# Optimization experiments

Measured on AMD Instinct MI355X. Metric: run time of the kernel, lower is better.

Reference implementation:

```python
import jax, jax.numpy as jnp
import numpy as np

NUM_EMBED = 1024
NUM_HEADS = 16
BLOCK_SIZE = 2048


def setup_inputs() -> dict:
    key = jax.random.key(0)
    k1, k2, k3, k4, k5 = jax.random.split(key, 5)
    C = NUM_EMBED
    s = 1.0 / np.sqrt(C)
    x = jax.random.normal(k1, (2, BLOCK_SIZE, C), dtype=jnp.float32)
    # nn.Linear params: weight (out,in), bias (out,)
    w_attn = jax.random.uniform(k2, (3 * C, C), minval=-s, maxval=s, dtype=jnp.float32)
    b_attn = jax.random.uniform(k3, (3 * C,), minval=-s, maxval=s, dtype=jnp.float32)
    w_proj = jax.random.uniform(k4, (C, C), minval=-s, maxval=s, dtype=jnp.float32)
    b_proj = jax.random.uniform(k5, (C,), minval=-s, maxval=s, dtype=jnp.float32)
    return {"x": x, "w_attn": w_attn, "b_attn": b_attn, "w_proj": w_proj, "b_proj": b_proj}


def reference(x, w_attn, b_attn, w_proj, b_proj):
    B, T, C = x.shape
    H = NUM_HEADS
    D = C // H
    kqv = jnp.einsum('btc,oc->bto', x, w_attn) + b_attn  # (B,T,3C)
    # Original code splits as K, Q, V in that order.
    K, Q, V = jnp.split(kqv, 3, axis=2)
    K = K.reshape(B, T, H, D).transpose(0, 2, 1, 3)  # (B,H,T,D)
    Q = Q.reshape(B, T, H, D).transpose(0, 2, 1, 3)
    V = V.reshape(B, T, H, D).transpose(0, 2, 1, 3)
    aff = jnp.einsum('bhqd,bhkd->bhqk', Q, K) * (D ** -0.5)  # (B,H,T,T)
    causal = jnp.tril(jnp.ones((T, T), dtype=bool))
    aff = jnp.where(causal[None, None], aff, jnp.float32(-jnp.inf))
    wei = jax.nn.softmax(aff, axis=-1)
    attn = jnp.einsum('bhqk,bhkd->bhqd', wei, V)
    attn = attn.transpose(0, 2, 1, 3).reshape(B, T, C)
    out = jnp.einsum('btc,oc->bto', attn, w_proj) + b_proj
    return out
```

## Files before the change

### kernel.cpp

```cpp
#include <hip/hip_runtime.h>
#include <hip/hip_bf16.h>
#include <cstdint>

typedef __attribute__((ext_vector_type(8))) short bf16x8;
typedef __attribute__((ext_vector_type(4))) float f32x4;
typedef __attribute__((ext_vector_type(4))) uint16_t u16x4;

__device__ __forceinline__ uint16_t f2b(float f) {
  union { float f; uint32_t i; } v; v.f = f;
  return (uint16_t)((v.i + 0x7FFFu + ((v.i >> 16) & 1u)) >> 16);
}

#define GLDS16(g, l) __builtin_amdgcn_global_load_lds( \
    (const __attribute__((address_space(1))) void*)(g), \
    (__attribute__((address_space(3))) void*)(l), 16, 0, 0)

__global__ __launch_bounds__(256) void cvt_all(
    const float* __restrict__ x, const float* __restrict__ wa, const float* __restrict__ wp,
    uint16_t* __restrict__ xb, uint16_t* __restrict__ wab, uint16_t* __restrict__ wpb) {
  const int i = (blockIdx.x * 256 + threadIdx.x) * 4;
  const float* src; uint16_t* dst; int off;
  if (i < 4194304)      { src = x;  dst = xb;  off = i; }
  else if (i < 7340032) { src = wa; dst = wab; off = i - 4194304; }
  else                  { src = wp; dst = wpb; off = i - 7340032; }
  const float4 v = *(const float4*)(src + off);
  u16x4 o;
  o.x = f2b(v.x); o.y = f2b(v.y); o.z = f2b(v.z); o.w = f2b(v.w);
  *(u16x4*)(dst + off) = o;
}

template <int BM, bool OUT_BF16>
__global__ __launch_bounds__(256) void gemm_bt_bias(
    const uint16_t* __restrict__ A, const uint16_t* __restrict__ B,
    const float* __restrict__ bias, void* __restrict__ Cv,
    int M, int N, int K) {
  constexpr int MI = BM / 32;
  constexpr int CA = BM / 16;
  constexpr int CPW = (2 * (CA + 8)) / 4;
  constexpr int CT_PITCH = OUT_BF16 ? 72 : 68;
  constexpr size_t CT_BYTES = (size_t)4 * (BM / 2) * CT_PITCH * (OUT_BF16 ? 2 : 4);
  constexpr size_t ST_BYTES = (size_t)(2 * (BM * 32 + 4096)) * 2;
  constexpr size_t LB = CT_BYTES > ST_BYTES ? CT_BYTES : ST_BYTES;
  __shared__ alignas(16) unsigned char ldsb[LB];
  uint16_t* lds = (uint16_t*)ldsb;
  const int offB0 = BM * 32;
  const int offA1 = BM * 32 + 4096;
  const int offB1 = 2 * BM * 32 + 4096;

  const int tid = threadIdx.x;
  const int wave = tid >> 6, lane = tid & 63;
  const int q4 = lane >> 4, l16 = lane & 15;
  const int wm = wave >> 1, wn = wave & 1;
  const long blockM = (long)blockIdx.y * BM;
  const long blockN = (long)blockIdx.x * 128;

  f32x4 acc[MI][4] = {};

  for (int k0 = 0; k0 < K; k0 += 64) {
#pragma unroll
    for (int c = 0; c < CPW; ++c) {
      const int id = c * 4 + wave;
      const uint16_t* mat; long rowBase; int a, kk, off;
      if (id < CA)               { mat = A; rowBase = blockM; a = id;            kk = k0;      off = 0; }
      else if (id < CA + 8)      { mat = B; rowBase = blockN; a = id - CA;       kk = k0;      off = offB0; }
      else if (id < 2 * CA + 8)  { mat = A; rowBase = blockM; a = id - CA - 8;   kk = k0 + 32; off = offA1; }
      else                       { mat = B; rowBase = blockN; a = id - 2*CA - 8; kk = k0 + 32; off = offB1; }
      const int flat = a * 64 + lane;
      const int row = flat >> 2, seg = flat & 3;
      GLDS16(mat + (rowBase + row) * (long)K + kk + seg * 8, lds + off + a * 512);
    }
    __syncthreads();
#pragma unroll
    for (int h = 0; h < 2; ++h) {
      const uint16_t* Ah = lds + (h ? offA1 : 0);
      const uint16_t* Bh = lds + (h ? offB1 : offB0);
      bf16x8 af[MI], bfr[4];
#pragma unroll
      for (int i = 0; i < MI; ++i)
        af[i] = *(const bf16x8*)&Ah[(wm * (BM / 2) + i * 16 + l16) * 32 + q4 * 8];
#pragma unroll
      for (int j = 0; j < 4; ++j)
        bfr[j] = *(const bf16x8*)&Bh[(wn * 64 + j * 16 + l16) * 32 + q4 * 8];
#pragma unroll
      for (int i = 0; i < MI; ++i)
#pragma unroll
        for (int j = 0; j < 4; ++j)
          acc[i][j] = __builtin_amdgcn_mfma_f32_16x16x32_bf16(af[i], bfr[j], acc[i][j], 0, 0, 0);
    }
    __syncthreads();
  }

  if (OUT_BF16) {
    uint16_t* ct = lds + wave * (BM / 2) * 72;
#pragma unroll
    for (int j = 0; j < 4; ++j) {
      const float bv = bias[blockN + wn * 64 + j * 16 + l16];
#pragma unroll
      for (int i = 0; i < MI; ++i)
#pragma unroll
        for (int r = 0; r < 4; ++r)
          ct[(i * 16 + q4 * 4 + r) * 72 + j * 16 + l16] = f2b(acc[i][j][r] + bv);
    }
    __syncthreads();
    uint16_t* Cb = (uint16_t*)Cv;
#pragma unroll
    for (int st = 0; st < BM / 16; ++st) {
      const int flat = st * 64 + lane;
      const int row = flat >> 3, seg = flat & 7;
      const bf16x8 v = *(const bf16x8*)&ct[row * 72 + seg * 8];
      *(bf16x8*)&Cb[(blockM + wm * (BM / 2) + row) * (long)N + blockN + wn * 64 + seg * 8] = v;
    }
  } else {
    float* ct = (float*)ldsb + wave * (BM / 2) * 68;
#pragma unroll
    for (int j = 0; j < 4; ++j) {
      const float bv = bias[blockN + wn * 64 + j * 16 + l16];
#pragma unroll
      for (int i = 0; i < MI; ++i)
#pragma unroll
        for (int r = 0; r < 4; ++r)
          ct[(i * 16 + q4 * 4 + r) * 68 + j * 16 + l16] = acc[i][j][r] + bv;
    }
    __syncthreads();
    float* Cb = (float*)Cv;
#pragma unroll
    for (int st = 0; st < BM / 8; ++st) {
      const int flat = st * 64 + lane;
      const int row = flat >> 4, seg = flat & 15;
      const f32x4 v = *(const f32x4*)&ct[row * 68 + seg * 4];
      *(f32x4*)&Cb[(blockM + wm * (BM / 2) + row) * (long)N + blockN + wn * 64 + seg * 4] = v;
    }
  }
}

__global__ __launch_bounds__(256, 2) void attn_flash(
    const uint16_t* __restrict__ kqv, uint16_t* __restrict__ attn) {
  constexpr int T = 2048, C = 1024, C3 = 3072;
  __shared__ uint16_t KP[128 * 72];
  __shared__ uint16_t Vt[64 * 136];
  uint32_t* VtW = (uint32_t*)Vt;

  const int tid = threadIdx.x;
  const int wave = tid >> 6, lane = tid & 63;
  const int q4 = lane >> 4, l16 = lane & 15;
  const int p = blockIdx.x >> 5, bh = blockIdx.x & 31;
  const int b = bh >> 4, h = bh & 15;
  const size_t base = (size_t)b * T * C3;
  const int hD = h * 64;

  uint16_t* Pt = &KP[wave * 2176];

  const int tr = tid >> 3, kch = tid & 7;
  const float sc = 0.125f * 1.4426950408889634f;

  for (int ss = 0; ss < 2; ++ss) {
    const int qb = ss ? p : 31 - p;
    const int nkt = (qb >> 1) + 1;
    const int qrow = qb * 64 + wave * 16 + l16;
    const bf16x8 qf0 = *(const bf16x8*)&kqv[base + (size_t)qrow * C3 + C + hD + q4 * 8];
    const bf16x8 qf1 = *(const bf16x8*)&kqv[base + (size_t)qrow * C3 + C + hD + 32 + q4 * 8];

    f32x4 o[4] = {};
    float m_i = -1e30f, l_i = 0.f;

    bf16x8 pk[4], pv0[2], pv1[2];
#pragma unroll
    for (int rr = 0; rr < 4; ++rr)
      pk[rr] = *(const bf16x8*)&kqv[base + (size_t)(rr * 32 + tr) * C3 + hD + kch * 8];
#pragma unroll
    for (int s2 = 0; s2 < 2; ++s2) {
      const size_t g = base + (size_t)(2 * (s2 * 32 + tr)) * C3 + 2 * C + hD + kch * 8;
      pv0[s2] = *(const bf16x8*)&kqv[g];
      pv1[s2] = *(const bf16x8*)&kqv[g + C3];
    }

    for (int kt = 0; kt < nkt; ++kt) {
      const int kbase = kt * 128;
      __syncthreads();
#pragma unroll
      for (int rr = 0; rr < 4; ++rr)
        *(bf16x8*)&KP[(rr * 32 + tr) * 72 + kch * 8] = pk[rr];
#pragma unroll
      for (int s2 = 0; s2 < 2; ++s2) {
        const int colw = ((s2 * 32 + tr) + 8 * kch) & 63;
        const uint32_t* a0 = (const uint32_t*)&pv0[s2];
        const uint32_t* a1 = (const uint32_t*)&pv1[s2];
#pragma unroll
        for (int i = 0; i < 8; ++i) {
          const uint32_t w = (i & 1)
              ? __builtin_amdgcn_perm(a1[i >> 1], a0[i >> 1], 0x07060302u)
              : __builtin_amdgcn_perm(a1[i >> 1], a0[i >> 1], 0x05040100u);
          VtW[(kch * 8 + i) * 68 + colw] = w;
        }
      }
      __syncthreads();
      if (kt + 1 < nkt) {
        const int kb = kbase + 128;
#pragma unroll
        for (int rr = 0; rr < 4; ++rr)
          pk[rr] = *(const bf16x8*)&kqv[base + (size_t)(kb + rr * 32 + tr) * C3 + hD + kch * 8];
#pragma unroll
        for (int s2 = 0; s2 < 2; ++s2) {
          const size_t g = base + (size_t)(kb + 2 * (s2 * 32 + tr)) * C3 + 2 * C + hD + kch * 8;
          pv0[s2] = *(const bf16x8*)&kqv[g];
          pv1[s2] = *(const bf16x8*)&kqv[g + C3];
        }
      }
      f32x4 s[8];
#pragma unroll
      for (int nk = 0; nk < 8; ++nk) {
        f32x4 z = {};
        const bf16x8 kf0 = *(const bf16x8*)&KP[(nk * 16 + l16) * 72 + q4 * 8];
        const bf16x8 kf1 = *(const bf16x8*)&KP[(nk * 16 + l16) * 72 + 32 + q4 * 8];
        z = __builtin_amdgcn_mfma_f32_16x16x32_bf16(kf0, qf0, z, 0, 0, 0);
        z = __builtin_amdgcn_mfma_f32_16x16x32_bf16(kf1, qf1, z, 0, 0, 0);
        s[nk] = z;
      }
      if (kbase + 127 > qb * 64 + wave * 16) {
#pragma unroll
        for (int nk = 0; nk < 8; ++nk) {
          const int key0 = kbase + nk * 16 + q4 * 4;
#pragma unroll
          for (int r = 0; r < 4; ++r)
            s[nk][r] = (key0 + r <= qrow) ? s[nk][r] : -1e30f;
        }
      }
      float mloc = s[0][0];
#pragma unroll
      for (int nk = 0; nk < 8; ++nk)
#pragma unroll
        for (int r = 0; r < 4; ++r) mloc = fmaxf(mloc, s[nk][r]);
      mloc = fmaxf(mloc, __shfl_xor(mloc, 16, 64));
      mloc = fmaxf(mloc, __shfl_xor(mloc, 32, 64));
      const float mnew = fmaxf(m_i, mloc * sc);
      const float alpha = exp2f(m_i - mnew);
      const bool mchg = mnew > m_i;
      m_i = mnew;
      float rs = 0.f;
#pragma unroll
      for (int nk = 0; nk < 8; ++nk)
#pragma unroll
        for (int r = 0; r < 4; ++r) {
          const float pe = exp2f(fmaf(s[nk][r], sc, -mnew));
          s[nk][r] = pe;
          rs += pe;
        }
      rs += __shfl_xor(rs, 16, 64);
      rs += __shfl_xor(rs, 32, 64);
      l_i = l_i * alpha + rs;
      if (__any(mchg)) {
#pragma unroll
        for (int r = 0; r < 4; ++r) {
          const float ar = __shfl(alpha, q4 * 4 + r, 64);
#pragma unroll
          for (int d4 = 0; d4 < 4; ++d4) o[d4][r] *= ar;
        }
      }
      __syncthreads();
#pragma unroll
      for (int nk = 0; nk < 8; ++nk) {
        union { __hip_bfloat162 h2; uint32_t u; } c01, c23;
        c01.h2 = __float22bfloat162_rn(make_float2(s[nk][0], s[nk][1]));
        c23.h2 = __float22bfloat162_rn(make_float2(s[nk][2], s[nk][3]));
        uint2 pkw; pkw.x = c01.u; pkw.y = c23.u;
        *(uint2*)&Pt[l16 * 136 + nk * 16 + q4 * 4] = pkw;
      }
      __syncthreads();
#pragma unroll
      for (int ks = 0; ks < 4; ++ks) {
        const bf16x8 pf = *(const bf16x8*)&Pt[l16 * 136 + ks * 32 + q4 * 8];
#pragma unroll
        for (int d4 = 0; d4 < 4; ++d4) {
          const int d = d4 * 16 + l16;
          const int col = (ks * 32 + q4 * 8 + 16 * (d >> 3)) & 127;
          const bf16x8 vf = *(const bf16x8*)&Vt[d * 136 + col];
          o[d4] = __builtin_amdgcn_mfma_f32_16x16x32_bf16(pf, vf, o[d4], 0, 0, 0);
        }
      }
    }
    const size_t obase = (size_t)b * T * C;
    const float linv = 1.0f / l_i;
#pragma unroll
    for (int r = 0; r < 4; ++r) {
      const float lr = __shfl(linv, q4 * 4 + r, 64);
      const int q = qb * 64 + wave * 16 + q4 * 4 + r;
      const size_t rowoff = obase + (size_t)q * C + hD;
#pragma unroll
      for (int d4 = 0; d4 < 4; ++d4)
        attn[rowoff + d4 * 16 + l16] = f2b(o[d4][r] * lr);
    }
  }
}

extern "C" void kernel_launch(void* const* d_in, const int* in_sizes, int n_in,
                              void* d_out, int out_size, void* d_ws, size_t ws_size,
                              hipStream_t stream) {
  const float* x      = (const float*)d_in[0];
  const float* w_attn = (const float*)d_in[1];
  const float* b_attn = (const float*)d_in[2];
  const float* w_proj = (const float*)d_in[3];
  const float* b_proj = (const float*)d_in[4];
  float* out = (float*)d_out;

  uint16_t* xb    = (uint16_t*)d_ws;
  uint16_t* wab   = xb  + (size_t)4096 * 1024;
  uint16_t* wpb   = wab + (size_t)3072 * 1024;
  uint16_t* kqv   = wpb + (size_t)1024 * 1024;
  uint16_t* attnb = kqv + (size_t)4096 * 3072;

  dim3 blk(256, 1, 1);
  hipLaunchKernelGGL(cvt_all, dim3(8192), blk, 0, stream, x, w_attn, w_proj, xb, wab, wpb);

  hipLaunchKernelGGL((gemm_bt_bias<128, true>), dim3(3072 / 128, 4096 / 128, 1), blk, 0, stream,
                     xb, wab, b_attn, (void*)kqv, 4096, 3072, 1024);
  hipLaunchKernelGGL(attn_flash, dim3(512, 1, 1), blk, 0, stream, kqv, attnb);
  hipLaunchKernelGGL((gemm_bt_bias<64, false>), dim3(1024 / 128, 4096 / 64, 1), blk, 0, stream,
                     attnb, wpb, b_proj, (void*)out, 4096, 1024, 1024);
}
```

Before: 194.8 us.

## Rewrite flash attention with 32x32 MFMA, register P, per-block causal skipping

New measurement: 201.1 us. +3.3%, slower.

```diff
diff --git a/kernel.cpp b/kernel.cpp
--- a/kernel.cpp
+++ b/kernel.cpp
@@ -4,11 +4,18 @@
 
 typedef __attribute__((ext_vector_type(8))) short bf16x8;
 typedef __attribute__((ext_vector_type(4))) float f32x4;
+typedef __attribute__((ext_vector_type(16))) float f32x16;
 typedef __attribute__((ext_vector_type(4))) uint16_t u16x4;
 
 __device__ __forceinline__ uint16_t f2b(float f) {
   union { float f; uint32_t i; } v; v.f = f;
   return (uint16_t)((v.i + 0x7FFFu + ((v.i >> 16) & 1u)) >> 16);
+}
+
+__device__ __forceinline__ uint32_t pkbf(float a, float b) {
+  union { __hip_bfloat162 h2; uint32_t u; } c;
+  c.h2 = __float22bfloat162_rn(make_float2(a, b));
+  return c.u;
 }
 
 #define GLDS16(g, l) __builtin_amdgcn_global_load_lds( \
@@ -142,153 +149,169 @@
 
   const int tid = threadIdx.x;
   const int wave = tid >> 6, lane = tid & 63;
-  const int q4 = lane >> 4, l16 = lane & 15;
-  const int p = blockIdx.x >> 5, bh = blockIdx.x & 31;
+  const int l32 = lane & 31, hh = lane >> 5;
+  const int sidx = blockIdx.x >> 5, bh = blockIdx.x & 31;
   const int b = bh >> 4, h = bh & 15;
   const size_t base = (size_t)b * T * C3;
   const int hD = h * 64;
 
-  uint16_t* Pt = &KP[wave * 2176];
-
   const int tr = tid >> 3, kch = tid & 7;
   const float sc = 0.125f * 1.4426950408889634f;
 
-  for (int ss = 0; ss < 2; ++ss) {
-    const int qb = ss ? p : 31 - p;
-    const int nkt = (qb >> 1) + 1;
-    const int qrow = qb * 64 + wave * 16 + l16;
-    const bf16x8 qf0 = *(const bf16x8*)&kqv[base + (size_t)qrow * C3 + C + hD + q4 * 8];
-    const bf16x8 qf1 = *(const bf16x8*)&kqv[base + (size_t)qrow * C3 + C + hD + 32 + q4 * 8];
-
-    f32x4 o[4] = {};
-    float m_i = -1e30f, l_i = 0.f;
-
-    bf16x8 pk[4], pv0[2], pv1[2];
+  const int qb = (sidx < 8) ? (15 - sidx) : (sidx - 8);
+  const int nkt = qb + 1;
+  const int qrow = qb * 128 + wave * 32 + l32;
+
+  bf16x8 qf[4];
+#pragma unroll
+  for (int m = 0; m < 4; ++m)
+    qf[m] = *(const bf16x8*)&kqv[base + (size_t)qrow * C3 + C + hD + m * 16 + hh * 8];
+
+  f32x16 o[2] = {};
+  float m_i = -1e30f, l_i = 0.f;
+
+  bf16x8 pk[4], pv0[2], pv1[2];
+#pragma unroll
+  for (int rr = 0; rr < 4; ++rr)
+    pk[rr] = *(const bf16x8*)&kqv[base + (size_t)(rr * 32 + tr) * C3 + hD + kch * 8];
+#pragma unroll
+  for (int s2 = 0; s2 < 2; ++s2) {
+    const size_t g = base + (size_t)(2 * (s2 * 32 + tr)) * C3 + 2 * C + hD + kch * 8;
+    pv0[s2] = *(const bf16x8*)&kqv[g];
+    pv1[s2] = *(const bf16x8*)&kqv[g + C3];
+  }
+
+  for (int kt = 0; kt < nkt; ++kt) {
+    __syncthreads();
 #pragma unroll
     for (int rr = 0; rr < 4; ++rr)
-      pk[rr] = *(const bf16x8*)&kqv[base + (size_t)(rr * 32 + tr) * C3 + hD + kch * 8];
+      *(bf16x8*)&KP[(rr * 32 + tr) * 72 + kch * 8] = pk[rr];
 #pragma unroll
     for (int s2 = 0; s2 < 2; ++s2) {
-      const size_t g = base + (size_t)(2 * (s2 * 32 + tr)) * C3 + 2 * C + hD + kch * 8;
-      pv0[s2] = *(const bf16x8*)&kqv[g];
-      pv1[s2] = *(const bf16x8*)&kqv[g + C3];
-    }
-
-    for (int kt = 0; kt < nkt; ++kt) {
-      const int kbase = kt * 128;
-      __syncthreads();
+      const int colw = ((s2 * 32 + tr) + 8 * kch) & 63;
+      const uint32_t* a0 = (const uint32_t*)&pv0[s2];
+      const uint32_t* a1 = (const uint32_t*)&pv1[s2];
+#pragma unroll
+      for (int i = 0; i < 8; ++i) {
+        const uint32_t w = (i & 1)
+            ? __builtin_amdgcn_perm(a1[i >> 1], a0[i >> 1], 0x07060302u)
+            : __builtin_amdgcn_perm(a1[i >> 1], a0[i >> 1], 0x05040100u);
+        VtW[(kch * 8 + i) * 68 + colw] = w;
+      }
+    }
+    __syncthreads();
+    if (kt + 1 < nkt) {
+      const int kb2 = (kt + 1) * 128;
 #pragma unroll
       for (int rr = 0; rr < 4; ++rr)
-        *(bf16x8*)&KP[(rr * 32 + tr) * 72 + kch * 8] = pk[rr];
+        pk[rr] = *(const bf16x8*)&kqv[base + (size_t)(kb2 + rr * 32 + tr) * C3 + hD + kch * 8];
 #pragma unroll
       for (int s2 = 0; s2 < 2; ++s2) {
-        const int colw = ((s2 * 32 + tr) + 8 * kch) & 63;
-        const uint32_t* a0 = (const uint32_t*)&pv0[s2];
-        const uint32_t* a1 = (const uint32_t*)&pv1[s2];
-#pragma unroll
-        for (int i = 0; i < 8; ++i) {
-          const uint32_t w = (i & 1)
-              ? __builtin_amdgcn_perm(a1[i >> 1], a0[i >> 1], 0x07060302u)
-              : __builtin_amdgcn_perm(a1[i >> 1], a0[i >> 1], 0x05040100u);
-          VtW[(kch * 8 + i) * 68 + colw] = w;
+        const size_t g = base + (size_t)(kb2 + 2 * (s2 * 32 + tr)) * C3 + 2 * C + hD + kch * 8;
+        pv0[s2] = *(const bf16x8*)&kqv[g];
+        pv1[s2] = *(const bf16x8*)&kqv[g + C3];
+      }
+    }
+
+    const int kbmax = (kt == qb) ? wave : 3;
+
+    f32x16 z[4];
+#pragma unroll
+    for (int kb = 0; kb < 4; ++kb) {
+      if (kb <= kbmax) {
+        f32x16 zz = {};
+#pragma unroll
+        for (int m = 0; m < 4; ++m) {
+          const bf16x8 kf = *(const bf16x8*)&KP[(kb * 32 + l32) * 72 + m * 16 + hh * 8];
+          zz = __builtin_amdgcn_mfma_f32_32x32x16_bf16(kf, qf[m], zz, 0, 0, 0);
         }
-      }
-      __syncthreads();
-      if (kt + 1 < nkt) {
-        const int kb = kbase + 128;
-#pragma unroll
-        for (int rr = 0; rr < 4; ++rr)
-          pk[rr] = *(const bf16x8*)&kqv[base + (size_t)(kb + rr * 32 + tr) * C3 + hD + kch * 8];
-#pragma unroll
-        for (int s2 = 0; s2 < 2; ++s2) {
-          const size_t g = base + (size_t)(kb + 2 * (s2 * 32 + tr)) * C3 + 2 * C + hD + kch * 8;
-          pv0[s2] = *(const bf16x8*)&kqv[g];
-          pv1[s2] = *(const bf16x8*)&kqv[g + C3];
+        if (kt == qb && kb == wave) {
+#pragma unroll
+          for (int r = 0; r < 16; ++r) {
+            const int keyl = (r & 3) + 8 * (r >> 2) + 4 * hh;
+            if (keyl > l32) zz[r] = -1e30f;
+          }
         }
-      }
-      f32x4 s[8];
-#pragma unroll
-      for (int nk = 0; nk < 8; ++nk) {
-        f32x4 z = {};
-        const bf16x8 kf0 = *(const bf16x8*)&KP[(nk * 16 + l16) * 72 + q4 * 8];
-        const bf16x8 kf1 = *(const bf16x8*)&KP[(nk * 16 + l16) * 72 + 32 + q4 * 8];
-        z = __builtin_amdgcn_mfma_f32_16x16x32_bf16(kf0, qf0, z, 0, 0, 0);
-        z = __builtin_amdgcn_mfma_f32_16x16x32_bf16(kf1, qf1, z, 0, 0, 0);
-        s[nk] = z;
-      }
-      if (kbase + 127 > qb * 64 + wave * 16) {
-#pragma unroll
-        for (int nk = 0; nk < 8; ++nk) {
-          const int key0 = kbase + nk * 16 + q4 * 4;
-#pragma unroll
-          for (int r = 0; r < 4; ++r)
-            s[nk][r] = (key0 + r <= qrow) ? s[nk][r] : -1e30f;
-        }
-      }
-      float mloc = s[0][0];
-#pragma unroll
-      for (int nk = 0; nk < 8; ++nk)
-#pragma unroll
-        for (int r = 0; r < 4; ++r) mloc = fmaxf(mloc, s[nk][r]);
-      mloc = fmaxf(mloc, __shfl_xor(mloc, 16, 64));
-      mloc = fmaxf(mloc, __shfl_xor(mloc, 32, 64));
-      const float mnew = fmaxf(m_i, mloc * sc);
-      const float alpha = exp2f(m_i - mnew);
-      const bool mchg = mnew > m_i;
-      m_i = mnew;
-      float rs = 0.f;
-#pragma unroll
-      for (int nk = 0; nk < 8; ++nk)
-#pragma unroll
-        for (int r = 0; r < 4; ++r) {
-          const float pe = exp2f(fmaf(s[nk][r], sc, -mnew));
-          s[nk][r] = pe;
+        z[kb] = zz;
+      }
+    }
+
+    float mloc = -1e30f;
+#pragma unroll
+    for (int kb = 0; kb < 4; ++kb)
+      if (kb <= kbmax)
+#pragma unroll
+        for (int r = 0; r < 16; ++r) mloc = fmaxf(mloc, z[kb][r]);
+    mloc = fmaxf(mloc, __shfl_xor(mloc, 32, 64));
+    const float mnew = fmaxf(m_i, mloc * sc);
+    const float alpha = exp2f(m_i - mnew);
+    const bool mchg = mnew > m_i;
+    m_i = mnew;
+    float rs = 0.f;
+#pragma unroll
+    for (int kb = 0; kb < 4; ++kb)
+      if (kb <= kbmax)
+#pragma unroll
+        for (int r = 0; r < 16; ++r) {
+          const float pe = exp2f(fmaf(z[kb][r], sc, -mnew));
+          z[kb][r] = pe;
           rs += pe;
         }
-      rs += __shfl_xor(rs, 16, 64);
-      rs += __shfl_xor(rs, 32, 64);
-      l_i = l_i * alpha + rs;
-      if (__any(mchg)) {
-#pragma unroll
-        for (int r = 0; r < 4; ++r) {
-          const float ar = __shfl(alpha, q4 * 4 + r, 64);
-#pragma unroll
-          for (int d4 = 0; d4 < 4; ++d4) o[d4][r] *= ar;
+    rs += __shfl_xor(rs, 32, 64);
+    l_i = l_i * alpha + rs;
+    if (__any(mchg)) {
+#pragma unroll
+      for (int r = 0; r < 16; ++r) {
+        const float ar = __shfl(alpha, (r & 3) + 8 * (r >> 2) + 4 * hh, 64);
+        o[0][r] *= ar;
+        o[1][r] *= ar;
+      }
+    }
+
+#pragma unroll
+    for (int kb = 0; kb < 4; ++kb) {
+      if (kb <= kbmax) {
+        uint32_t x0 = pkbf(z[kb][0], z[kb][1]),   x1 = pkbf(z[kb][2], z[kb][3]);
+        uint32_t y0 = pkbf(z[kb][4], z[kb][5]),   y1 = pkbf(z[kb][6], z[kb][7]);
+        uint32_t x2 = pkbf(z[kb][8], z[kb][9]),   x3 = pkbf(z[kb][10], z[kb][11]);
+        uint32_t y2 = pkbf(z[kb][12], z[kb][13]), y3 = pkbf(z[kb][14], z[kb][15]);
+        const uint32_t s0 = hh ? x0 : y0, s1 = hh ? x1 : y1;
+        const uint32_t s2 = hh ? x2 : y2, s3 = hh ? x3 : y3;
+        const uint32_t t0 = __shfl_xor(s0, 32, 64), t1 = __shfl_xor(s1, 32, 64);
+        const uint32_t t2 = __shfl_xor(s2, 32, 64), t3 = __shfl_xor(s3, 32, 64);
+#pragma unroll
+        for (int cc = 0; cc < 2; ++cc) {
+          const int c = 2 * kb + cc;
+          union { bf16x8 v; uint32_t w[4]; } pa;
+          if (cc == 0) {
+            pa.w[0] = hh ? t0 : x0; pa.w[1] = hh ? t1 : x1;
+            pa.w[2] = hh ? y0 : t0; pa.w[3] = hh ? y1 : t1;
+          } else {
+            pa.w[0] = hh ? t2 : x2; pa.w[1] = hh ? t3 : x3;
+            pa.w[2] = hh ? y2 : t2; pa.w[3] = hh ? y3 : t3;
+          }
+#pragma unroll
+          for (int db = 0; db < 2; ++db) {
+            const int d = db * 32 + l32;
+            const int col = (c * 16 + hh * 8 + 16 * (d >> 3)) & 127;
+            const bf16x8 vf = *(const bf16x8*)&Vt[d * 136 + col];
+            o[db] = __builtin_amdgcn_mfma_f32_32x32x16_bf16(pa.v, vf, o[db], 0, 0, 0);
+          }
         }
       }
-      __syncthreads();
-#pragma unroll
-      for (int nk = 0; nk < 8; ++nk) {
-        union { __hip_bfloat162 h2; uint32_t u; } c01, c23;
-        c01.h2 = __float22bfloat162_rn(make_float2(s[nk][0], s[nk][1]));
-        c23.h2 = __float22bfloat162_rn(make_float2(s[nk][2], s[nk][3]));
-        uint2 pkw; pkw.x = c01.u; pkw.y = c23.u;
-        *(uint2*)&Pt[l16 * 136 + nk * 16 + q4 * 4] = pkw;
-      }
-      __syncthreads();
-#pragma unroll
-      for (int ks = 0; ks < 4; ++ks) {
-        const bf16x8 pf = *(const bf16x8*)&Pt[l16 * 136 + ks * 32 + q4 * 8];
-#pragma unroll
-        for (int d4 = 0; d4 < 4; ++d4) {
-          const int d = d4 * 16 + l16;
-          const int col = (ks * 32 + q4 * 8 + 16 * (d >> 3)) & 127;
-          const bf16x8 vf = *(const bf16x8*)&Vt[d * 136 + col];
-          o[d4] = __builtin_amdgcn_mfma_f32_16x16x32_bf16(pf, vf, o[d4], 0, 0, 0);
-        }
-      }
-    }
-    const size_t obase = (size_t)b * T * C;
-    const float linv = 1.0f / l_i;
-#pragma unroll
-    for (int r = 0; r < 4; ++r) {
-      const float lr = __shfl(linv, q4 * 4 + r, 64);
-      const int q = qb * 64 + wave * 16 + q4 * 4 + r;
-      const size_t rowoff = obase + (size_t)q * C + hD;
-#pragma unroll
-      for (int d4 = 0; d4 < 4; ++d4)
-        attn[rowoff + d4 * 16 + l16] = f2b(o[d4][r] * lr);
-    }
+    }
+  }
+
+  const size_t obase = (size_t)b * T * C;
+  const float linv = 1.0f / l_i;
+#pragma unroll
+  for (int r = 0; r < 16; ++r) {
+    const int ql = (r & 3) + 8 * (r >> 2) + 4 * hh;
+    const float lr = __shfl(linv, ql, 64);
+    const int q = qb * 128 + wave * 32 + ql;
+    const size_t rowoff = obase + (size_t)q * C + hD;
+    attn[rowoff + l32] = f2b(o[0][r] * lr);
+    attn[rowoff + 32 + l32] = f2b(o[1][r] * lr);
   }
 }
 
```
